# Kernel tuning notes

Measured on AMD Instinct MI355X. Metric: run time of the kernel, lower is better.

Reference implementation:

```python
import jax, jax.numpy as jnp
import numpy as np

N = 100000
E = 1600000
G = 64  # number of graphs in batch
IN_DIM = 256
HID = 64
HEADS = 4
NUM_DOMAINS = 2
NEG_SLOPE = 0.2


def setup_inputs() -> dict:
    key = jax.random.key(0)
    ks = jax.random.split(key, 16)
    x = jax.random.normal(ks[0], (N, IN_DIM), dtype=jnp.float32)
    edge_index = jax.random.randint(ks[1], (2, E), 0, N, dtype=jnp.int64)
    batch = jnp.sort(jax.random.randint(ks[2], (N,), 0, G, dtype=jnp.int64))
    s = 1.0 / np.sqrt(IN_DIM)
    W1 = jax.random.uniform(ks[3], (IN_DIM, HEADS * HID), jnp.float32, -s, s)
    att_src1 = jax.random.normal(ks[4], (HEADS, HID), jnp.float32) * 0.1
    att_dst1 = jax.random.normal(ks[5], (HEADS, HID), jnp.float32) * 0.1
    b1 = jnp.zeros((HEADS * HID,), jnp.float32)
    s2 = 1.0 / np.sqrt(HEADS * HID)
    W2 = jax.random.uniform(ks[6], (HEADS * HID, HID), jnp.float32, -s2, s2)
    att_src2 = jax.random.normal(ks[7], (1, HID), jnp.float32) * 0.1
    att_dst2 = jax.random.normal(ks[8], (1, HID), jnp.float32) * 0.1
    b2 = jnp.zeros((HID,), jnp.float32)
    s3 = 1.0 / np.sqrt(HID)
    W3 = jax.random.uniform(ks[9], (HID, HID // 2), jnp.float32, -s3, s3)
    b3 = jnp.zeros((HID // 2,), jnp.float32)
    s4 = 1.0 / np.sqrt(HID // 2)
    W4 = jax.random.uniform(ks[10], (HID // 2, NUM_DOMAINS), jnp.float32, -s4, s4)
    b4 = jnp.zeros((NUM_DOMAINS,), jnp.float32)
    return dict(x=x, edge_index=edge_index, batch=batch,
                W1=W1, att_src1=att_src1, att_dst1=att_dst1, b1=b1,
                W2=W2, att_src2=att_src2, att_dst2=att_dst2, b2=b2,
                W3=W3, b3=b3, W4=W4, b4=b4)


def gat_conv(x, src, dst, W, att_src, att_dst, bias, concat):
    # PyG GATConv (dropout inactive in eval mode)
    H, C = att_src.shape
    h = (x @ W).reshape(N, H, C)                      # [N,H,C]
    a_src = jnp.sum(h * att_src, axis=-1)             # [N,H]
    a_dst = jnp.sum(h * att_dst, axis=-1)             # [N,H]
    alpha = jax.nn.leaky_relu(a_src[src] + a_dst[dst], NEG_SLOPE)  # [E',H]
    amax = jax.ops.segment_max(alpha, dst, num_segments=N)
    alpha = jnp.exp(alpha - amax[dst])
    denom = jax.ops.segment_sum(alpha, dst, num_segments=N)
    alpha = alpha / (denom[dst] + 1e-16)              # segment softmax over incoming edges
    msg = h[src] * alpha[..., None]                   # [E',H,C]
    out = jax.ops.segment_sum(msg, dst, num_segments=N)  # [N,H,C]
    if concat:
        return out.reshape(N, H * C) + bias
    return out.mean(axis=1) + bias


def reference(x, edge_index, batch,
              W1, att_src1, att_dst1, b1,
              W2, att_src2, att_dst2, b2,
              W3, b3, W4, b4):
    # GRL is identity in forward
    loops = jnp.arange(N, dtype=edge_index.dtype)
    src = jnp.concatenate([edge_index[0], loops])  # add_self_loops (PyG default)
    dst = jnp.concatenate([edge_index[1], loops])
    h = jax.nn.elu(gat_conv(x, src, dst, W1, att_src1, att_dst1, b1, concat=True))
    h = gat_conv(h, src, dst, W2, att_src2, att_dst2, b2, concat=False)  # [N,HID]
    # global mean pool over graphs
    sums = jax.ops.segment_sum(h, batch, num_segments=G)
    cnt = jax.ops.segment_sum(jnp.ones((N,), h.dtype), batch, num_segments=G)
    graph_emb = sums / jnp.maximum(cnt, 1.0)[:, None]  # [G,HID]
    z = jax.nn.relu(graph_emb @ W3 + b3)
    logits = z @ W4 + b4                                # [G,NUM_DOMAINS]
    return logits
```

## Files before the change

kernel.cpp:

```cpp
#include <hip/hip_runtime.h>
#include <math.h>

#define N_NODES 100000
#define E_EDGES 1600000
#define E_TOT   (E_EDGES + N_NODES)
#define G_GRAPHS 64
#define IN_DIM 256
#define HID 64
#define HEADS 4
#define D1 256
#define NEG_SLOPE 0.2f
#define SCAN_B 1024

typedef float nfloat4 __attribute__((ext_vector_type(4)));
typedef unsigned short nus4 __attribute__((ext_vector_type(4)));
typedef short bf16x8 __attribute__((ext_vector_type(8)));
typedef float f32x4 __attribute__((ext_vector_type(4)));

__device__ __forceinline__ float bf2f(unsigned short u) {
    unsigned int t = ((unsigned int)u) << 16;
    return __builtin_bit_cast(float, t);
}
__device__ __forceinline__ unsigned short f2bf(float f) {
    unsigned int u = __builtin_bit_cast(unsigned int, f);
    u += 0x7FFF + ((u >> 16) & 1);
    return (unsigned short)(u >> 16);
}
__device__ __forceinline__ unsigned int pk2(float lo, float hi) {
    unsigned int ul = __builtin_bit_cast(unsigned int, lo) + 0x8000u;
    unsigned int uh = __builtin_bit_cast(unsigned int, hi) + 0x8000u;
    return __builtin_amdgcn_perm(uh, ul, 0x07060302u);
}

__device__ __forceinline__ void packW(const float* __restrict__ W,
                                      unsigned short* __restrict__ Wpk, int Nc, int t)
{
    int kg = t / Nc, n = t - kg * Nc;
    const float* p = W + (size_t)(kg * 8) * Nc + n;
    uint4 v;
    v.x = pk2(p[0],      p[Nc]);
    v.y = pk2(p[2 * Nc], p[3 * Nc]);
    v.z = pk2(p[4 * Nc], p[5 * Nc]);
    v.w = pk2(p[6 * Nc], p[7 * Nc]);
    *(uint4*)(Wpk + (size_t)t * 8) = v;
}
__global__ __launch_bounds__(256) void convW2x(const float* __restrict__ W1,
                                               unsigned short* __restrict__ Wpk1,
                                               const float* __restrict__ W2,
                                               unsigned short* __restrict__ Wpk2)
{
    int t = blockIdx.x * 256 + threadIdx.x;
    if (t < 32 * D1) packW(W1, Wpk1, D1, t);
    else if (t < 32 * D1 + 32 * HID) packW(W2, Wpk2, HID, t - 32 * D1);
}

template<int BN, bool ABF16, bool CFP8>
__global__ __launch_bounds__(256) void gemm_mfma(const void* __restrict__ Ain,
                                                 const unsigned short* __restrict__ Wpk,
                                                 void* __restrict__ C,
                                                 int Nc,
                                                 const float* __restrict__ att_src,
                                                 const float* __restrict__ att_dst,
                                                 float* __restrict__ a_srcO,
                                                 float* __restrict__ a_dstO,
                                                 int astride)
{
    constexpr int NCG = BN / 16;
    __shared__ unsigned short alds[2][4][128][8];
    const int tid = threadIdx.x;
    const int lane = tid & 63, wv = tid >> 6;
    const int qd = lane >> 4, c16 = lane & 15;
    const int bm = blockIdx.y * 128, bn = blockIdx.x * BN;

    f32x4 acc[2][NCG];
#pragma unroll
    for (int i = 0; i < 2; ++i)
#pragma unroll
        for (int j = 0; j < NCG; ++j) acc[i][j] = (f32x4){0.f, 0.f, 0.f, 0.f};

    const int ar = tid >> 1, akh = tid & 1;
    const int gm = bm + ar;
    const bool mv = gm < N_NODES;

    uint4 v0, v1;
    float4 f0, f1, f2, f3;
    if (ABF16) {
        const unsigned short* Ab = (const unsigned short*)Ain + (size_t)gm * 256 + akh * 16;
        v0 = mv ? *(const uint4*)Ab : make_uint4(0, 0, 0, 0);
        v1 = mv ? *(const uint4*)(Ab + 8) : make_uint4(0, 0, 0, 0);
    } else {
        const float* Af = (const float*)Ain + (size_t)gm * 256 + akh * 16;
        if (mv) { f0 = ((const float4*)Af)[0]; f1 = ((const float4*)Af)[1];
                  f2 = ((const float4*)Af)[2]; f3 = ((const float4*)Af)[3]; }
        else { f0 = f1 = f2 = f3 = make_float4(0.f, 0.f, 0.f, 0.f); }
    }

    for (int k0 = 0; k0 < 256; k0 += 32) {
        const int p = (k0 >> 5) & 1;
        if (ABF16) {
            *(uint4*)&alds[p][2 * akh][ar][0] = v0;
            *(uint4*)&alds[p][2 * akh + 1][ar][0] = v1;
        } else {
            uint4 p0 = make_uint4(pk2(f0.x, f0.y), pk2(f0.z, f0.w), pk2(f1.x, f1.y), pk2(f1.z, f1.w));
            uint4 p1 = make_uint4(pk2(f2.x, f2.y), pk2(f2.z, f2.w), pk2(f3.x, f3.y), pk2(f3.z, f3.w));
            *(uint4*)&alds[p][2 * akh][ar][0] = p0;
            *(uint4*)&alds[p][2 * akh + 1][ar][0] = p1;
        }
        __syncthreads();

        if (k0 + 32 < 256) {
            if (ABF16) {
                const unsigned short* Ab = (const unsigned short*)Ain + (size_t)gm * 256 + (k0 + 32) + akh * 16;
                v0 = mv ? *(const uint4*)Ab : make_uint4(0, 0, 0, 0);
                v1 = mv ? *(const uint4*)(Ab + 8) : make_uint4(0, 0, 0, 0);
            } else {
                const float* Af = (const float*)Ain + (size_t)gm * 256 + (k0 + 32) + akh * 16;
                if (mv) { f0 = ((const float4*)Af)[0]; f1 = ((const float4*)Af)[1];
                          f2 = ((const float4*)Af)[2]; f3 = ((const float4*)Af)[3]; }
            }
        }

        const unsigned short* Wq = Wpk + ((size_t)((k0 >> 3) + qd) * Nc + bn) * 8;
        bf16x8 af0 = *(const bf16x8*)&alds[p][qd][wv * 32 + c16][0];
        bf16x8 af1 = *(const bf16x8*)&alds[p][qd][wv * 32 + 16 + c16][0];
#pragma unroll
        for (int cg = 0; cg < NCG; ++cg) {
            bf16x8 bfr = *(const bf16x8*)(Wq + (size_t)(cg * 16 + c16) * 8);
            acc[0][cg] = __builtin_amdgcn_mfma_f32_16x16x32_bf16(af0, bfr, acc[0][cg], 0, 0, 0);
            acc[1][cg] = __builtin_amdgcn_mfma_f32_16x16x32_bf16(af1, bfr, acc[1][cg], 0, 0, 0);
        }
    }

    float sv[NCG], dv[NCG];
#pragma unroll
    for (int cg = 0; cg < NCG; ++cg) {
        sv[cg] = att_src[bn + cg * 16 + c16];
        dv[cg] = att_dst[bn + cg * 16 + c16];
    }
#pragma unroll
    for (int rg = 0; rg < 2; ++rg) {
#pragma unroll
        for (int reg = 0; reg < 4; ++reg) {
            const int m = bm + wv * 32 + rg * 16 + qd * 4 + reg;
#pragma unroll
            for (int hh = 0; hh < NCG / 4; ++hh) {
                float ps = 0.f, pd = 0.f;
#pragma unroll
                for (int cg = 4 * hh; cg < 4 * hh + 4; ++cg) {
                    ps += acc[rg][cg][reg] * sv[cg];
                    pd += acc[rg][cg][reg] * dv[cg];
                }
#pragma unroll
                for (int o = 1; o < 16; o <<= 1) { ps += __shfl_xor(ps, o); pd += __shfl_xor(pd, o); }
                if (c16 == 0 && m < N_NODES) {
                    a_srcO[m * astride + (bn >> 6) + hh] = ps;
                    a_dstO[m * astride + (bn >> 6) + hh] = pd;
                }
            }
            if (m < N_NODES) {
#pragma unroll
                for (int cg = 0; cg < NCG; ++cg) {
                    float val = acc[rg][cg][reg];
                    if (CFP8) {
                        unsigned int q = (unsigned int)__builtin_amdgcn_cvt_pk_fp8_f32(val, val, 0, false);
                        ((unsigned char*)C)[(size_t)m * Nc + bn + cg * 16 + c16] = (unsigned char)q;
                    } else {
                        ((unsigned short*)C)[(size_t)m * Nc + bn + cg * 16 + c16] = f2bf(val);
                    }
                }
            }
        }
    }
}

__global__ void edge_hist(const int* __restrict__ ei, int* __restrict__ deg,
                          int* __restrict__ rank)
{
    for (int e = blockIdx.x * blockDim.x + threadIdx.x; e < E_TOT; e += gridDim.x * blockDim.x) {
        int d = (e < E_EDGES) ? ei[E_EDGES + e] : (e - E_EDGES);
        rank[e] = atomicAdd(&deg[d], 1);
    }
}

__global__ __launch_bounds__(SCAN_B) void scan_block(const int* __restrict__ deg,
                                                     int* __restrict__ incl,
                                                     int* __restrict__ bsum, int n)
{
    __shared__ int s[SCAN_B];
    int i = blockIdx.x * SCAN_B + threadIdx.x;
    int v = (i < n) ? deg[i] : 0;
    s[threadIdx.x] = v;
    __syncthreads();
    for (int off = 1; off < SCAN_B; off <<= 1) {
        int t = (threadIdx.x >= off) ? s[threadIdx.x - off] : 0;
        __syncthreads();
        s[threadIdx.x] += t;
        __syncthreads();
    }
    if (i < n) incl[i] = s[threadIdx.x];
    if (threadIdx.x == SCAN_B - 1) bsum[blockIdx.x] = s[SCAN_B - 1];
}

__global__ void scan_bsum(const int* __restrict__ bsum, int* __restrict__ bex, int nb)
{
    __shared__ int s[128];
    int i = threadIdx.x;
    int v = (i < nb) ? bsum[i] : 0;
    s[i] = v;
    __syncthreads();
    for (int off = 1; off < 128; off <<= 1) {
        int t = (i >= off) ? s[i - off] : 0;
        __syncthreads();
        s[i] += t;
        __syncthreads();
    }
    if (i < nb) bex[i] = s[i] - v;
}

__global__ void finalize_off(const int* __restrict__ deg, const int* __restrict__ incl,
                             const int* __restrict__ bex, int* __restrict__ off, int n)
{
    int i = blockIdx.x * blockDim.x + threadIdx.x;
    if (i < n) off[i] = incl[i] - deg[i] + bex[i / SCAN_B];
}

__global__ void edge_scatter(const int* __restrict__ ei, const int* __restrict__ off,
                             const int* __restrict__ rank, int* __restrict__ csr_src)
{
    for (int e = blockIdx.x * blockDim.x + threadIdx.x; e < E_TOT; e += gridDim.x * blockDim.x) {
        int s = (e < E_EDGES) ? ei[e] : (e - E_EDGES);
        int d = (e < E_EDGES) ? ei[E_EDGES + e] : (e - E_EDGES);
        csr_src[off[d] + rank[e]] = s;
    }
}

__global__ __launch_bounds__(256) void agg1_kernel(const unsigned char* __restrict__ h1b,
                                                   const int* __restrict__ csr_src,
                                                   const int* __restrict__ off,
                                                   const int* __restrict__ deg,
                                                   const float* __restrict__ a_src,
                                                   const float* __restrict__ a_dst,
                                                   const float* __restrict__ b1,
                                                   unsigned short* __restrict__ hEb)
{
    __shared__ int s_sh[4][72];
    __shared__ __align__(16) float ex_sh[4][72][4];
    const int wv = threadIdx.x >> 6, lane = threadIdx.x & 63;
    const int n = blockIdx.x * 4 + wv;
    if (n >= N_NODES) return;
    const int h = lane >> 4;
    const int st = off[n], cnt = deg[n];
    const float4 ad4 = *(const float4*)(a_dst + (size_t)n * 4);

    float4 acc = make_float4(0.f, 0.f, 0.f, 0.f);
    float dsum = 0.f;
    const unsigned char* __restrict__ hb = h1b + lane * 4;

    for (int cb = 0; cb < cnt; cb += 64) {
        const int c0 = st + cb;
        const int m = (cnt - cb < 64) ? (cnt - cb) : 64;

        {
            int s_l = csr_src[c0 + ((lane < m) ? lane : 0)];
            float4 as4 = *(const float4*)(a_src + (size_t)s_l * 4);
            float e0 = as4.x + ad4.x, e1 = as4.y + ad4.y,
                  e2 = as4.z + ad4.z, e3 = as4.w + ad4.w;
            e0 = (e0 > 0.f) ? e0 : NEG_SLOPE * e0;
            e1 = (e1 > 0.f) ? e1 : NEG_SLOPE * e1;
            e2 = (e2 > 0.f) ? e2 : NEG_SLOPE * e2;
            e3 = (e3 > 0.f) ? e3 : NEG_SLOPE * e3;
            float4 exv;
            exv.x = __expf(e0); exv.y = __expf(e1);
            exv.z = __expf(e2); exv.w = __expf(e3);
            if (lane < m) {
                s_sh[wv][lane] = s_l;
                *(float4*)&ex_sh[wv][lane][0] = exv;
            }
            if (lane < 8) {
                s_sh[wv][m + lane] = csr_src[c0];
                *(float4*)&ex_sh[wv][m + lane][0] = make_float4(0.f, 0.f, 0.f, 0.f);
            }
        }

        const int m4 = (m + 3) & ~3;
        int   sR0 = s_sh[wv][0], sR1 = s_sh[wv][1], sR2 = s_sh[wv][2], sR3 = s_sh[wv][3];
        float eR0 = ex_sh[wv][0][h], eR1 = ex_sh[wv][1][h],
              eR2 = ex_sh[wv][2][h], eR3 = ex_sh[wv][3][h];
        unsigned int vR0 = *(const unsigned int*)(hb + (size_t)sR0 * D1);
        unsigned int vR1 = *(const unsigned int*)(hb + (size_t)sR1 * D1);
        unsigned int vR2 = *(const unsigned int*)(hb + (size_t)sR2 * D1);
        unsigned int vR3 = *(const unsigned int*)(hb + (size_t)sR3 * D1);
        for (int j = 0; j < m4; j += 4) {
            int   sN0 = s_sh[wv][j + 4], sN1 = s_sh[wv][j + 5],
                  sN2 = s_sh[wv][j + 6], sN3 = s_sh[wv][j + 7];
            float eN0 = ex_sh[wv][j + 4][h], eN1 = ex_sh[wv][j + 5][h],
                  eN2 = ex_sh[wv][j + 6][h], eN3 = ex_sh[wv][j + 7][h];
            unsigned int vN0 = *(const unsigned int*)(hb + (size_t)sN0 * D1);
            unsigned int vN1 = *(const unsigned int*)(hb + (size_t)sN1 * D1);
            unsigned int vN2 = *(const unsigned int*)(hb + (size_t)sN2 * D1);
            unsigned int vN3 = *(const unsigned int*)(hb + (size_t)sN3 * D1);

            dsum += eR0;
            acc.x += eR0 * __builtin_amdgcn_cvt_f32_fp8((int)vR0, 0);
            acc.y += eR0 * __builtin_amdgcn_cvt_f32_fp8((int)vR0, 1);
            acc.z += eR0 * __builtin_amdgcn_cvt_f32_fp8((int)vR0, 2);
            acc.w += eR0 * __builtin_amdgcn_cvt_f32_fp8((int)vR0, 3);
            dsum += eR1;
            acc.x += eR1 * __builtin_amdgcn_cvt_f32_fp8((int)vR1, 0);
            acc.y += eR1 * __builtin_amdgcn_cvt_f32_fp8((int)vR1, 1);
            acc.z += eR1 * __builtin_amdgcn_cvt_f32_fp8((int)vR1, 2);
            acc.w += eR1 * __builtin_amdgcn_cvt_f32_fp8((int)vR1, 3);
            dsum += eR2;
            acc.x += eR2 * __builtin_amdgcn_cvt_f32_fp8((int)vR2, 0);
            acc.y += eR2 * __builtin_amdgcn_cvt_f32_fp8((int)vR2, 1);
            acc.z += eR2 * __builtin_amdgcn_cvt_f32_fp8((int)vR2, 2);
            acc.w += eR2 * __builtin_amdgcn_cvt_f32_fp8((int)vR2, 3);
            dsum += eR3;
            acc.x += eR3 * __builtin_amdgcn_cvt_f32_fp8((int)vR3, 0);
            acc.y += eR3 * __builtin_amdgcn_cvt_f32_fp8((int)vR3, 1);
            acc.z += eR3 * __builtin_amdgcn_cvt_f32_fp8((int)vR3, 2);
            acc.w += eR3 * __builtin_amdgcn_cvt_f32_fp8((int)vR3, 3);

            sR0 = sN0; sR1 = sN1; sR2 = sN2; sR3 = sN3;
            eR0 = eN0; eR1 = eN1; eR2 = eN2; eR3 = eN3;
            vR0 = vN0; vR1 = vN1; vR2 = vN2; vR3 = vN3;
        }
    }

    const float inv = 1.f / (dsum + 1e-16f);
    float4 bb = *(const float4*)(b1 + lane * 4);
    float ox = acc.x * inv + bb.x;
    float oy = acc.y * inv + bb.y;
    float oz = acc.z * inv + bb.z;
    float ow = acc.w * inv + bb.w;
    ox = (ox > 0.f) ? ox : expm1f(ox);
    oy = (oy > 0.f) ? oy : expm1f(oy);
    oz = (oz > 0.f) ? oz : expm1f(oz);
    ow = (ow > 0.f) ? ow : expm1f(ow);
    nus4 ob = { f2bf(ox), f2bf(oy), f2bf(oz), f2bf(ow) };
    __builtin_nontemporal_store(ob, (nus4*)(hEb + (size_t)n * D1 + lane * 4));
}

__global__ __launch_bounds__(256) void agg2_node_kernel(const unsigned short* __restrict__ h2b,
                                                        const int* __restrict__ csr_src,
                                                        const int* __restrict__ off,
                                                        const int* __restrict__ deg,
                                                        const float* __restrict__ a_src,
                                                        const float* __restrict__ a_dst,
                                                        const float* __restrict__ b2,
                                                        float* __restrict__ h3)
{
    __shared__ int   s_sh[4][96];
    __shared__ float ex_sh[4][96];
    const int wv = threadIdx.x >> 6, lane = threadIdx.x & 63;
    const int n = blockIdx.x * 4 + wv;
    if (n >= N_NODES) return;
    const int q = lane >> 4, ql = lane & 15;
    const int f0 = ql * 4;
    const int st = off[n], cnt = deg[n];
    const float adn = a_dst[n];
    const unsigned short* __restrict__ hb = h2b + f0;

    float4 acc = make_float4(0.f, 0.f, 0.f, 0.f);
    float dsum = 0.f;

    for (int cb = 0; cb < cnt; cb += 64) {
        const int c0 = st + cb;
        const int m = (cnt - cb < 64) ? (cnt - cb) : 64;

        {
            int s_l = csr_src[c0 + ((lane < m) ? lane : 0)];
            float a = a_src[s_l] + adn;
            a = (a > 0.f) ? a : NEG_SLOPE * a;
            float ex = __expf(a);
            if (lane < m) { s_sh[wv][lane] = s_l; ex_sh[wv][lane] = ex; }
            int sb = __shfl(s_l, 0);
            if (lane < 32) { s_sh[wv][m + lane] = sb; ex_sh[wv][m + lane] = 0.f; }
        }

        const int m4 = (m + 3) & ~3;
        int   sA = s_sh[wv][q],      sB = s_sh[wv][q + 4],  sC = s_sh[wv][q + 8];
        float eA = ex_sh[wv][q],     eB = ex_sh[wv][q + 4], eC = ex_sh[wv][q + 8];
        ushort4 vA = *(const ushort4*)(hb + (size_t)sA * HID);
        ushort4 vB = *(const ushort4*)(hb + (size_t)sB * HID);
        ushort4 vC = *(const ushort4*)(hb + (size_t)sC * HID);
        for (int j = 0; j < m4; j += 4) {
            int   sD = s_sh[wv][j + 12 + q];
            float eD = ex_sh[wv][j + 12 + q];
            ushort4 vD = *(const ushort4*)(hb + (size_t)sD * HID);

            dsum += eA;
            acc.x += eA * bf2f(vA.x); acc.y += eA * bf2f(vA.y);
            acc.z += eA * bf2f(vA.z); acc.w += eA * bf2f(vA.w);

            sA = sB; eA = eB; vA = vB;
            sB = sC; eB = eC; vB = vC;
            sC = sD; eC = eD; vC = vD;
        }
    }

    dsum  += __shfl_xor(dsum, 16);  dsum  += __shfl_xor(dsum, 32);
    acc.x += __shfl_xor(acc.x, 16); acc.x += __shfl_xor(acc.x, 32);
    acc.y += __shfl_xor(acc.y, 16); acc.y += __shfl_xor(acc.y, 32);
    acc.z += __shfl_xor(acc.z, 16); acc.z += __shfl_xor(acc.z, 32);
    acc.w += __shfl_xor(acc.w, 16); acc.w += __shfl_xor(acc.w, 32);

    const float inv = 1.f / (dsum + 1e-16f);
    const float4 bb = *(const float4*)(b2 + f0);
    float4 v;
    v.x = acc.x * inv + bb.x;
    v.y = acc.y * inv + bb.y;
    v.z = acc.z * inv + bb.z;
    v.w = acc.w * inv + bb.w;
    if (q == 0)
        __builtin_nontemporal_store(*(nfloat4*)&v, (nfloat4*)(h3 + (size_t)n * HID + f0));
}

__global__ __launch_bounds__(256) void pool_kernel(const float* __restrict__ h3,
                                                   const int* __restrict__ batch,
                                                   float* __restrict__ pool,
                                                   float* __restrict__ cntg,
                                                   int per)
{
    const int w = blockIdx.x * 4 + (threadIdx.x >> 6);
    const int lane = threadIdx.x & 63;
    const int n0 = w * per;
    if (n0 >= N_NODES) return;
    const int n1 = (n0 + per < N_NODES) ? n0 + per : N_NODES;

    float accv = 0.f, c = 0.f;
    int gcur = batch[n0];
    for (int n = n0; n < n1; ++n) {
        float v = h3[(size_t)n * HID + lane];
        int g = batch[n];
        if (g != gcur) {
#if defined(__AMDGCN__)
            unsafeAtomicAdd(&pool[gcur * HID + lane], accv);
            if (lane == 0) unsafeAtomicAdd(&cntg[gcur], c);
#else
            atomicAdd(&pool[gcur * HID + lane], accv);
            if (lane == 0) atomicAdd(&cntg[gcur], c);
#endif
            accv = 0.f; c = 0.f; gcur = g;
        }
        accv += v; c += 1.f;
    }
#if defined(__AMDGCN__)
    unsafeAtomicAdd(&pool[gcur * HID + lane], accv);
    if (lane == 0) unsafeAtomicAdd(&cntg[gcur], c);
#else
    atomicAdd(&pool[gcur * HID + lane], accv);
    if (lane == 0) atomicAdd(&cntg[gcur], c);
#endif
}

__global__ __launch_bounds__(64) void head_kernel(const float* __restrict__ pool,
                                                  const float* __restrict__ cntg,
                                                  const float* __restrict__ W3,
                                                  const float* __restrict__ b3,
                                                  const float* __restrict__ W4,
                                                  const float* __restrict__ b4,
                                                  float* __restrict__ out)
{
    const int g = blockIdx.x;
    const int lane = threadIdx.x;
    const float invc = 1.f / fmaxf(cntg[g], 1.f);
    float z = 0.f;
    if (lane < 32) {
        z = b3[lane];
        for (int k = 0; k < HID; ++k)
            z += pool[g * HID + k] * invc * W3[k * 32 + lane];
        z = fmaxf(z, 0.f);
    }
    float p0 = (lane < 32) ? z * W4[lane * 2 + 0] : 0.f;
    float p1 = (lane < 32) ? z * W4[lane * 2 + 1] : 0.f;
#pragma unroll
    for (int o = 1; o < 32; o <<= 1) { p0 += __shfl_xor(p0, o); p1 += __shfl_xor(p1, o); }
    if (lane == 0) { out[g * 2 + 0] = b4[0] + p0; out[g * 2 + 1] = b4[1] + p1; }
}

extern "C" void kernel_launch(void* const* d_in, const int* in_sizes, int n_in,
                              void* d_out, int out_size, void* d_ws, size_t ws_size,
                              hipStream_t stream)
{
    const float* x     = (const float*)d_in[0];
    const int*   ei    = (const int*)d_in[1];
    const int*   batch = (const int*)d_in[2];
    const float* W1    = (const float*)d_in[3];
    const float* as1w  = (const float*)d_in[4];
    const float* ad1w  = (const float*)d_in[5];
    const float* b1    = (const float*)d_in[6];
    const float* W2    = (const float*)d_in[7];
    const float* as2w  = (const float*)d_in[8];
    const float* ad2w  = (const float*)d_in[9];
    const float* b2    = (const float*)d_in[10];
    const float* W3    = (const float*)d_in[11];
    const float* b3    = (const float*)d_in[12];
    const float* W4    = (const float*)d_in[13];
    const float* b4    = (const float*)d_in[14];
    float* out = (float*)d_out;

    char* ws = (char*)d_ws;
    size_t o = 0;
    auto alloc = [&](size_t bytes) -> void* {
        void* p = ws + o;
        o += (bytes + 255) & ~(size_t)255;
        return p;
    };
    unsigned char*  h1b = (unsigned char*)alloc((size_t)N_NODES * D1);
    unsigned short* hEb = (unsigned short*)alloc((size_t)N_NODES * D1 * 2);
    unsigned short* h2b = (unsigned short*)alloc((size_t)N_NODES * HID * 2);
    float* h3   = (float*)alloc((size_t)N_NODES * HID * 4);
    float* a_s1 = (float*)alloc((size_t)N_NODES * 4 * 4);
    float* a_d1 = (float*)alloc((size_t)N_NODES * 4 * 4);
    float* a_s2 = (float*)alloc((size_t)N_NODES * 4);
    float* a_d2 = (float*)alloc((size_t)N_NODES * 4);
    char*  zbase  = (char*)alloc((size_t)N_NODES * 4 + G_GRAPHS * HID * 4 + G_GRAPHS * 4 + 1024);
    int*   deg    = (int*)zbase;
    float* pool   = (float*)(zbase + (((size_t)N_NODES * 4 + 255) & ~(size_t)255));
    float* cntg   = (float*)((char*)pool + (((size_t)G_GRAPHS * HID * 4 + 255) & ~(size_t)255));
    size_t zspan  = (char*)(cntg + G_GRAPHS) - zbase;
    int*   incl   = (int*)alloc((size_t)N_NODES * 4);
    int*   offv   = (int*)alloc((size_t)N_NODES * 4);
    int*   rank   = (int*)alloc((size_t)E_TOT * 4);
    int*   bsum   = (int*)alloc(128 * 4);
    int*   bex    = (int*)alloc(128 * 4);
    int*   csr    = (int*)alloc((size_t)E_TOT * 4);
    unsigned short* Wpk1 = (unsigned short*)alloc((size_t)32 * D1 * 8 * 2);
    unsigned short* Wpk2 = (unsigned short*)alloc((size_t)32 * HID * 8 * 2);

    (void)hipMemsetAsync(zbase, 0, zspan, stream);

    const int nblk_nodes = (N_NODES + 3) / 4;
    const int nscan = (N_NODES + SCAN_B - 1) / SCAN_B;
    const int nrowblk = (N_NODES + 127) / 128;

    convW2x<<<(32 * D1 + 32 * HID + 255) / 256, 256, 0, stream>>>(W1, Wpk1, W2, Wpk2);

    gemm_mfma<128, false, true><<<dim3(2, nrowblk), 256, 0, stream>>>(
        x, Wpk1, h1b, D1, as1w, ad1w, a_s1, a_d1, 4);

    edge_hist<<<4096, 256, 0, stream>>>(ei, deg, rank);
    scan_block<<<nscan, SCAN_B, 0, stream>>>(deg, incl, bsum, N_NODES);
    scan_bsum<<<1, 128, 0, stream>>>(bsum, bex, nscan);
    finalize_off<<<(N_NODES + 255) / 256, 256, 0, stream>>>(deg, incl, bex, offv, N_NODES);
    edge_scatter<<<4096, 256, 0, stream>>>(ei, offv, rank, csr);

    agg1_kernel<<<nblk_nodes, 256, 0, stream>>>(h1b, csr, offv, deg, a_s1, a_d1, b1, hEb);

    gemm_mfma<64, true, false><<<dim3(1, nrowblk), 256, 0, stream>>>(
        hEb, Wpk2, h2b, HID, as2w, ad2w, a_s2, a_d2, 1);

    agg2_node_kernel<<<nblk_nodes, 256, 0, stream>>>(h2b, csr, offv, deg, a_s2, a_d2, b2, h3);

    const int npool_blk = 512;
    const int per = (N_NODES + npool_blk * 4 - 1) / (npool_blk * 4);
    pool_kernel<<<npool_blk, 256, 0, stream>>>(h3, batch, pool, cntg, per);

    head_kernel<<<G_GRAPHS, 64, 0, stream>>>(pool, cntg, W3, b3, W4, b4, out);
}
```

Baseline: 552.0 us.

## Replace LDS-staged GEMM with direct-register MFMA loading full output width per wave

```diff
diff --git a/kernel.cpp b/kernel.cpp
--- a/kernel.cpp
+++ b/kernel.cpp
@@ -54,119 +54,98 @@
     else if (t < 32 * D1 + 32 * HID) packW(W2, Wpk2, HID, t - 32 * D1);
 }
 
-template<int BN, bool ABF16, bool CFP8>
-__global__ __launch_bounds__(256) void gemm_mfma(const void* __restrict__ Ain,
-                                                 const unsigned short* __restrict__ Wpk,
-                                                 void* __restrict__ C,
-                                                 int Nc,
-                                                 const float* __restrict__ att_src,
-                                                 const float* __restrict__ att_dst,
-                                                 float* __restrict__ a_srcO,
-                                                 float* __restrict__ a_dstO,
-                                                 int astride)
-{
-    constexpr int NCG = BN / 16;
-    __shared__ unsigned short alds[2][4][128][8];
-    const int tid = threadIdx.x;
-    const int lane = tid & 63, wv = tid >> 6;
+template<int NC, bool ABF16, bool CFP8>
+__global__ __launch_bounds__(256) void gemm_direct(const void* __restrict__ Ain,
+                                                   const unsigned short* __restrict__ Wpk,
+                                                   void* __restrict__ C,
+                                                   const float* __restrict__ att_src,
+                                                   const float* __restrict__ att_dst,
+                                                   float* __restrict__ a_srcO,
+                                                   float* __restrict__ a_dstO,
+                                                   int astride)
+{
+    constexpr int NCG = NC / 16;
+    const int lane = threadIdx.x & 63, wv = threadIdx.x >> 6;
     const int qd = lane >> 4, c16 = lane & 15;
-    const int bm = blockIdx.y * 128, bn = blockIdx.x * BN;
-
-    f32x4 acc[2][NCG];
-#pragma unroll
-    for (int i = 0; i < 2; ++i)
-#pragma unroll
-        for (int j = 0; j < NCG; ++j) acc[i][j] = (f32x4){0.f, 0.f, 0.f, 0.f};
-
-    const int ar = tid >> 1, akh = tid & 1;
-    const int gm = bm + ar;
+    const int r0 = blockIdx.x * 64 + wv * 16;
+    const int gm = r0 + c16;
     const bool mv = gm < N_NODES;
 
-    uint4 v0, v1;
-    float4 f0, f1, f2, f3;
+    f32x4 acc[NCG];
+#pragma unroll
+    for (int j = 0; j < NCG; ++j) acc[j] = (f32x4){0.f, 0.f, 0.f, 0.f};
+
+    uint4 ua;
+    float4 fa0, fa1;
     if (ABF16) {
-        const unsigned short* Ab = (const unsigned short*)Ain + (size_t)gm * 256 + akh * 16;
-        v0 = mv ? *(const uint4*)Ab : make_uint4(0, 0, 0, 0);
-        v1 = mv ? *(const uint4*)(Ab + 8) : make_uint4(0, 0, 0, 0);
+        const unsigned short* Ab = (const unsigned short*)Ain + (size_t)gm * 256 + qd * 8;
+        ua = mv ? *(const uint4*)Ab : make_uint4(0, 0, 0, 0);
     } else {
-        const float* Af = (const float*)Ain + (size_t)gm * 256 + akh * 16;
-        if (mv) { f0 = ((const float4*)Af)[0]; f1 = ((const float4*)Af)[1];
-                  f2 = ((const float4*)Af)[2]; f3 = ((const float4*)Af)[3]; }
-        else { f0 = f1 = f2 = f3 = make_float4(0.f, 0.f, 0.f, 0.f); }
+        const float* Af = (const float*)Ain + (size_t)gm * 256 + qd * 8;
+        if (mv) { fa0 = ((const float4*)Af)[0]; fa1 = ((const float4*)Af)[1]; }
+        else { fa0 = fa1 = make_float4(0.f, 0.f, 0.f, 0.f); }
     }
 
     for (int k0 = 0; k0 < 256; k0 += 32) {
-        const int p = (k0 >> 5) & 1;
+        bf16x8 af;
         if (ABF16) {
-            *(uint4*)&alds[p][2 * akh][ar][0] = v0;
-            *(uint4*)&alds[p][2 * akh + 1][ar][0] = v1;
+            af = __builtin_bit_cast(bf16x8, ua);
         } else {
-            uint4 p0 = make_uint4(pk2(f0.x, f0.y), pk2(f0.z, f0.w), pk2(f1.x, f1.y), pk2(f1.z, f1.w));
-            uint4 p1 = make_uint4(pk2(f2.x, f2.y), pk2(f2.z, f2.w), pk2(f3.x, f3.y), pk2(f3.z, f3.w));
-            *(uint4*)&alds[p][2 * akh][ar][0] = p0;
-            *(uint4*)&alds[p][2 * akh + 1][ar][0] = p1;
-        }
-        __syncthreads();
-
+            uint4 w;
+            w.x = pk2(fa0.x, fa0.y); w.y = pk2(fa0.z, fa0.w);
+            w.z = pk2(fa1.x, fa1.y); w.w = pk2(fa1.z, fa1.w);
+            af = __builtin_bit_cast(bf16x8, w);
+        }
         if (k0 + 32 < 256) {
             if (ABF16) {
-                const unsigned short* Ab = (const unsigned short*)Ain + (size_t)gm * 256 + (k0 + 32) + akh * 16;
-                v0 = mv ? *(const uint4*)Ab : make_uint4(0, 0, 0, 0);
-                v1 = mv ? *(const uint4*)(Ab + 8) : make_uint4(0, 0, 0, 0);
+                const unsigned short* Ab = (const unsigned short*)Ain + (size_t)gm * 256 + (k0 + 32) + qd * 8;
+                ua = mv ? *(const uint4*)Ab : make_uint4(0, 0, 0, 0);
             } else {
-                const float* Af = (const float*)Ain + (size_t)gm * 256 + (k0 + 32) + akh * 16;
-                if (mv) { f0 = ((const float4*)Af)[0]; f1 = ((const float4*)Af)[1];
-                          f2 = ((const float4*)Af)[2]; f3 = ((const float4*)Af)[3]; }
+                const float* Af = (const float*)Ain + (size_t)gm * 256 + (k0 + 32) + qd * 8;
+                if (mv) { fa0 = ((const float4*)Af)[0]; fa1 = ((const float4*)Af)[1]; }
             }
         }
-
-        const unsigned short* Wq = Wpk + ((size_t)((k0 >> 3) + qd) * Nc + bn) * 8;
-        bf16x8 af0 = *(const bf16x8*)&alds[p][qd][wv * 32 + c16][0];
-        bf16x8 af1 = *(const bf16x8*)&alds[p][qd][wv * 32 + 16 + c16][0];
+        const unsigned short* Wq = Wpk + (size_t)((k0 >> 3) + qd) * NC * 8;
 #pragma unroll
         for (int cg = 0; cg < NCG; ++cg) {
             bf16x8 bfr = *(const bf16x8*)(Wq + (size_t)(cg * 16 + c16) * 8);
-            acc[0][cg] = __builtin_amdgcn_mfma_f32_16x16x32_bf16(af0, bfr, acc[0][cg], 0, 0, 0);
-            acc[1][cg] = __builtin_amdgcn_mfma_f32_16x16x32_bf16(af1, bfr, acc[1][cg], 0, 0, 0);
+            acc[cg] = __builtin_amdgcn_mfma_f32_16x16x32_bf16(af, bfr, acc[cg], 0, 0, 0);
         }
     }
 
     float sv[NCG], dv[NCG];
 #pragma unroll
     for (int cg = 0; cg < NCG; ++cg) {
-        sv[cg] = att_src[bn + cg * 16 + c16];
-        dv[cg] = att_dst[bn + cg * 16 + c16];
-    }
-#pragma unroll
-    for (int rg = 0; rg < 2; ++rg) {
-#pragma unroll
-        for (int reg = 0; reg < 4; ++reg) {
-            const int m = bm + wv * 32 + rg * 16 + qd * 4 + reg;
-#pragma unroll
-            for (int hh = 0; hh < NCG / 4; ++hh) {
-                float ps = 0.f, pd = 0.f;
-#pragma unroll
-                for (int cg = 4 * hh; cg < 4 * hh + 4; ++cg) {
-                    ps += acc[rg][cg][reg] * sv[cg];
-                    pd += acc[rg][cg][reg] * dv[cg];
-                }
-#pragma unroll
-                for (int o = 1; o < 16; o <<= 1) { ps += __shfl_xor(ps, o); pd += __shfl_xor(pd, o); }
-                if (c16 == 0 && m < N_NODES) {
-                    a_srcO[m * astride + (bn >> 6) + hh] = ps;
-                    a_dstO[m * astride + (bn >> 6) + hh] = pd;
-                }
+        sv[cg] = att_src[cg * 16 + c16];
+        dv[cg] = att_dst[cg * 16 + c16];
+    }
+#pragma unroll
+    for (int reg = 0; reg < 4; ++reg) {
+        const int m = r0 + qd * 4 + reg;
+#pragma unroll
+        for (int hh = 0; hh < NCG / 4; ++hh) {
+            float ps = 0.f, pd = 0.f;
+#pragma unroll
+            for (int cg = 4 * hh; cg < 4 * hh + 4; ++cg) {
+                ps += acc[cg][reg] * sv[cg];
+                pd += acc[cg][reg] * dv[cg];
             }
-            if (m < N_NODES) {
-#pragma unroll
-                for (int cg = 0; cg < NCG; ++cg) {
-                    float val = acc[rg][cg][reg];
-                    if (CFP8) {
-                        unsigned int q = (unsigned int)__builtin_amdgcn_cvt_pk_fp8_f32(val, val, 0, false);
-                        ((unsigned char*)C)[(size_t)m * Nc + bn + cg * 16 + c16] = (unsigned char)q;
-                    } else {
-                        ((unsigned short*)C)[(size_t)m * Nc + bn + cg * 16 + c16] = f2bf(val);
-                    }
+#pragma unroll
+            for (int o = 1; o < 16; o <<= 1) { ps += __shfl_xor(ps, o); pd += __shfl_xor(pd, o); }
+            if (c16 == 0 && m < N_NODES) {
+                a_srcO[m * astride + hh] = ps;
+                a_dstO[m * astride + hh] = pd;
+            }
+        }
+        if (m < N_NODES) {
+#pragma unroll
+            for (int cg = 0; cg < NCG; ++cg) {
+                float val = acc[cg][reg];
+                if (CFP8) {
+                    unsigned int q8 = (unsigned int)__builtin_amdgcn_cvt_pk_fp8_f32(val, val, 0, false);
+                    ((unsigned char*)C)[(size_t)m * NC + cg * 16 + c16] = (unsigned char)q8;
+                } else {
+                    ((unsigned short*)C)[(size_t)m * NC + cg * 16 + c16] = f2bf(val);
                 }
             }
         }
@@ -533,12 +512,12 @@
 
     const int nblk_nodes = (N_NODES + 3) / 4;
     const int nscan = (N_NODES + SCAN_B - 1) / SCAN_B;
-    const int nrowblk = (N_NODES + 127) / 128;
+    const int ngemm = (N_NODES + 63) / 64;
 
     convW2x<<<(32 * D1 + 32 * HID + 255) / 256, 256, 0, stream>>>(W1, Wpk1, W2, Wpk2);
 
-    gemm_mfma<128, false, true><<<dim3(2, nrowblk), 256, 0, stream>>>(
-        x, Wpk1, h1b, D1, as1w, ad1w, a_s1, a_d1, 4);
+    gemm_direct<D1, false, true><<<ngemm, 256, 0, stream>>>(
+        x, Wpk1, h1b, as1w, ad1w, a_s1, a_d1, 4);
 
     edge_hist<<<4096, 256, 0, stream>>>(ei, deg, rank);
     scan_block<<<nscan, SCAN_B, 0, stream>>>(deg, incl, bsum, N_NODES);
@@ -548,8 +527,8 @@
 
     agg1_kernel<<<nblk_nodes, 256, 0, stream>>>(h1b, csr, offv, deg, a_s1, a_d1, b1, hEb);
 
-    gemm_mfma<64, true, false><<<dim3(1, nrowblk), 256, 0, stream>>>(
-        hEb, Wpk2, h2b, HID, as2w, ad2w, a_s2, a_d2, 1);
+    gemm_direct<HID, true, false><<<ngemm, 256, 0, stream>>>(
+        hEb, Wpk2, h2b, as2w, ad2w, a_s2, a_d2, 1);
 
     agg2_node_kernel<<<nblk_nodes, 256, 0, stream>>>(h2b, csr, offv, deg, a_s2, a_d2, b2, h3);
 
```

Measured after the change: 574.0 us. 4.0% more time.
